# Kernel optimization log

Measured on AMD Instinct MI355X. Metric: run time of the kernel, lower is better.

The kernel has to match this reference:

```python
import jax, jax.numpy as jnp
import numpy as np
from jax import lax

SEQ, BATCH, IN, HID, OUT = 168, 4096, 24, 64, 9


def _uniform(key, shape, scale):
    return jax.random.uniform(key, shape, jnp.float32, -scale, scale)


def setup_inputs() -> dict:
    key = jax.random.key(0)
    ks = jax.random.split(key, 12)
    s = 1.0 / np.sqrt(HID)  # PyTorch LSTM/Linear init scale
    return {
        "x": jax.random.normal(ks[0], (SEQ, BATCH, IN), jnp.float32),
        # layer 0 LSTM (PyTorch gate order: i, f, g, o stacked along dim 0)
        "W_ih0": _uniform(ks[1], (4 * HID, IN), s),
        "W_hh0": _uniform(ks[2], (4 * HID, HID), s),
        "b_ih0": _uniform(ks[3], (4 * HID,), s),
        "b_hh0": _uniform(ks[4], (4 * HID,), s),
        # layer 1 LSTM
        "W_ih1": _uniform(ks[5], (4 * HID, HID), s),
        "W_hh1": _uniform(ks[6], (4 * HID, HID), s),
        "b_ih1": _uniform(ks[7], (4 * HID,), s),
        "b_hh1": _uniform(ks[8], (4 * HID,), s),
        # linear head
        "W_out": _uniform(ks[9], (OUT, HID), s),
        "b_out": _uniform(ks[10], (OUT,), s),
    }


def _lstm_layer(x, W_ih, W_hh, b_ih, b_hh):
    # x: [S, B, D]; returns hidden states [S, B, H]
    H = W_hh.shape[1]
    B = x.shape[1]
    # precompute input projections for all timesteps: [S, B, 4H]
    xg = jnp.einsum('sbd,gd->sbg', x, W_ih) + b_ih + b_hh

    def step(carry, xg_t):
        h, c = carry
        g = xg_t + h @ W_hh.T  # [B, 4H]
        i, f, gc, o = jnp.split(g, 4, axis=-1)
        c = jax.nn.sigmoid(f) * c + jax.nn.sigmoid(i) * jnp.tanh(gc)
        h = jax.nn.sigmoid(o) * jnp.tanh(c)
        return (h, c), h

    init = (jnp.zeros((B, H), x.dtype), jnp.zeros((B, H), x.dtype))
    _, hs = lax.scan(step, init, xg)
    return hs


def reference(x, W_ih0, W_hh0, b_ih0, b_hh0, W_ih1, W_hh1, b_ih1, b_hh1, W_out, b_out):
    h = _lstm_layer(x, W_ih0, W_hh0, b_ih0, b_hh0)   # [S, B, H]
    h = _lstm_layer(h, W_ih1, W_hh1, b_ih1, b_hh1)   # [S, B, H]
    out = jnp.einsum('sbh,oh->sbo', h, W_out) + b_out  # [S, B, OUT]
    return out
```

## Files before the change

### kernel.cpp

```cpp
#include <hip/hip_runtime.h>
#include <hip/hip_bf16.h>
#include <math.h>

#define SEQ   168
#define BATCH 4096
#define NOUT  9
#define NBLK  256

typedef short bf16x8 __attribute__((ext_vector_type(8)));
typedef float f32x4  __attribute__((ext_vector_type(4)));

#define MFMA(a,b,c) __builtin_amdgcn_mfma_f32_16x16x32_bf16((a),(b),(c),0,0,0)

static __device__ __forceinline__ float bf2f(unsigned short h){
    unsigned int u = ((unsigned int)h) << 16;
    return __builtin_bit_cast(float, u);
}
static __device__ __forceinline__ unsigned short f2bf(float f){
    return __builtin_bit_cast(unsigned short, __float2bfloat16(f));
}
static __device__ __forceinline__ void splitf(float f, unsigned short& hi, unsigned short& lo){
    hi = f2bf(f);
    float r = f - bf2f(hi);
    lo = (unsigned short)(__builtin_bit_cast(unsigned int, r) >> 16);
}
static __device__ __forceinline__ float sigf(float x){
    return __builtin_amdgcn_rcpf(1.0f + __expf(-x));
}
static __device__ __forceinline__ float tanhf_(float x){
    float r = __builtin_amdgcn_rcpf(1.0f + __expf(2.0f * x));
    return fmaf(-2.0f, r, 1.0f);
}
static __device__ __forceinline__ bf16x8 ldfrag(const unsigned short* p){
    const uint4 q = *reinterpret_cast<const uint4*>(p);
    return __builtin_bit_cast(bf16x8, q);
}

static __device__ __forceinline__ void gbar(int* cnt, int* phs, int* done,
                                            int tickval, int& ph, int lane){
    asm volatile("s_waitcnt lgkmcnt(0)" ::: "memory");
    if (lane == 0){
        int old = __hip_atomic_fetch_add(cnt, 1, __ATOMIC_ACQ_REL,
                                         __HIP_MEMORY_SCOPE_WORKGROUP);
        if (old == 3){
            *cnt = 0;
            __hip_atomic_store(done, tickval, __ATOMIC_RELEASE,
                               __HIP_MEMORY_SCOPE_WORKGROUP);
            __hip_atomic_store(phs, ph ^ 1, __ATOMIC_RELEASE,
                               __HIP_MEMORY_SCOPE_WORKGROUP);
        }
    }
    while (__hip_atomic_load(phs, __ATOMIC_ACQUIRE,
                             __HIP_MEMORY_SCOPE_WORKGROUP) == ph)
        __builtin_amdgcn_s_sleep(1);
    ph ^= 1;
}
static __device__ __forceinline__ void wait_ge(int* done, int need){
    if (__hip_atomic_load(done, __ATOMIC_ACQUIRE, __HIP_MEMORY_SCOPE_WORKGROUP) >= need) return;
    do { __builtin_amdgcn_s_sleep(1); }
    while (__hip_atomic_load(done, __ATOMIC_ACQUIRE, __HIP_MEMORY_SCOPE_WORKGROUP) < need);
}

__global__ __launch_bounds__(512, 2)
void lstm_fused(const float* __restrict__ x,
                const float* __restrict__ Wih0, const float* __restrict__ Whh0,
                const float* __restrict__ bih0, const float* __restrict__ bhh0,
                const float* __restrict__ Wih1, const float* __restrict__ Whh1,
                const float* __restrict__ bih1, const float* __restrict__ bhh1,
                const float* __restrict__ Wout, const float* __restrict__ bout,
                float* __restrict__ out)
{
    __shared__ __align__(16) unsigned short sXH[2][16][72];
    __shared__ __align__(16) unsigned short sH0H[2][16][72];
    __shared__ __align__(16) unsigned short sH1H[2][16][72];
    __shared__ int sync[8];

    const int tid  = threadIdx.x;
    const int half = tid >> 8;
    const int w2   = (tid >> 6) & 3;
    const int l    = tid & 63;
    const int lr   = l & 15;
    const int g    = l >> 4;
    const int r0   = blockIdx.x * 16;
    const int cg   = w2 * 16 + lr;

    if (tid < 8) sync[tid] = (tid >= 4) ? -1 : 0;

    for (int i = tid; i < (int)(2*16*72/2); i += 512){
        ((unsigned int*)sXH)[i]  = 0u;
        ((unsigned int*)sH0H)[i] = 0u;
        ((unsigned int*)sH1H)[i] = 0u;
    }
    __syncthreads();
    if (tid < 96){
        const float4 v = *reinterpret_cast<const float4*>(&x[(size_t)r0 * 24 + tid * 4]);
        const int row = (tid * 4) / 24, col = (tid * 4) % 24;
        ushort4 w = { f2bf(v.x), f2bf(v.y), f2bf(v.z), f2bf(v.w) };
        *reinterpret_cast<ushort4*>(&sXH[0][row][col]) = w;
    }
    __syncthreads();

    if (half == 0){
        bf16x8 B0H[4][3], B0L[4][3];
        #pragma unroll
        for (int gt = 0; gt < 4; ++gt){
            const int c = gt * 64 + cg;
            bf16x8 bh = {0,0,0,0,0,0,0,0}, bl = {0,0,0,0,0,0,0,0};
            if (g < 3){
                const float* pw = &Wih0[c * 24 + g * 8];
                #pragma unroll
                for (int j = 0; j < 8; ++j){ unsigned short hh, ll; splitf(pw[j], hh, ll); bh[j]=(short)hh; bl[j]=(short)ll; }
            }
            B0H[gt][0] = bh; B0L[gt][0] = bl;
            #pragma unroll
            for (int ks = 0; ks < 2; ++ks){
                bf16x8 ch, cl;
                const float* pw = &Whh0[c * 64 + ks * 32 + g * 8];
                #pragma unroll
                for (int j = 0; j < 8; ++j){ unsigned short hh, ll; splitf(pw[j], hh, ll); ch[j]=(short)hh; cl[j]=(short)ll; }
                B0H[gt][1+ks] = ch; B0L[gt][1+ks] = cl;
            }
        }
        float b0[4];
        #pragma unroll
        for (int gt = 0; gt < 4; ++gt) b0[gt] = bih0[gt*64 + cg] + bhh0[gt*64 + cg];

        const int oc = lr;
        bf16x8 WoH[2], WoL[2];
        #pragma unroll
        for (int tt = 0; tt < 2; ++tt){
            bf16x8 bh = {0,0,0,0,0,0,0,0}, bl = {0,0,0,0,0,0,0,0};
            if (oc < NOUT){
                const float* pw = &Wout[oc * 64 + tt * 32 + g * 8];
                #pragma unroll
                for (int j = 0; j < 8; ++j){ unsigned short hh, ll; splitf(pw[j], hh, ll); bh[j]=(short)hh; bl[j]=(short)ll; }
            }
            WoH[tt] = bh; WoL[tt] = bl;
        }
        const float bo0 = (oc < NOUT) ? bout[oc] : 0.f;
        float* houtp = out + (size_t)(r0 + g * 4) * NOUT + oc;

        const float* xfp = x + ((size_t)BATCH + r0) * 24 + tid * 4;
        float c0[4] = {0,0,0,0};
        int ph = 0;
        for (int t = 0; t < SEQ + 2; ++t){
            const int p = t & 1;
            const bool cmp = (t < SEQ);
            const bool ldx = (tid < 96) && (t + 1 < SEQ);
            float4 pref;
            if (ldx){ pref = *reinterpret_cast<const float4*>(xfp); xfp += (size_t)BATCH * 24; }

            unsigned short hh[4];
            if (cmp){
                const bf16x8 AxH = ldfrag(&sXH[p][lr][g*8]);
                bf16x8 A0H[2];
                #pragma unroll
                for (int ks = 0; ks < 2; ++ks)
                    A0H[ks] = ldfrag(&sH0H[p][lr][ks*32 + g*8]);

                f32x4 a0[4];
                #pragma unroll
                for (int gt = 0; gt < 4; ++gt){ f32x4 a = {b0[gt],b0[gt],b0[gt],b0[gt]}; a0[gt] = a; }
                #pragma unroll
                for (int gt = 0; gt < 4; ++gt) a0[gt] = MFMA(AxH, B0H[gt][0], a0[gt]);
                #pragma unroll
                for (int gt = 0; gt < 4; ++gt) a0[gt] = MFMA(AxH, B0L[gt][0], a0[gt]);
                #pragma unroll
                for (int ks = 0; ks < 2; ++ks){
                    #pragma unroll
                    for (int gt = 0; gt < 4; ++gt) a0[gt] = MFMA(A0H[ks], B0H[gt][1+ks], a0[gt]);
                    #pragma unroll
                    for (int gt = 0; gt < 4; ++gt) a0[gt] = MFMA(A0H[ks], B0L[gt][1+ks], a0[gt]);
                }
                #pragma unroll
                for (int i = 0; i < 4; ++i){
                    const float ig = sigf(a0[0][i]);
                    const float fg = sigf(a0[1][i]);
                    const float gg = tanhf_(a0[2][i]);
                    const float og = sigf(a0[3][i]);
                    c0[i] = fg * c0[i] + ig * gg;
                    hh[i] = f2bf(og * tanhf_(c0[i]));
                }
            }
            if (ldx){
                const int row = (tid * 4) / 24, col = (tid * 4) % 24;
                ushort4 w = { f2bf(pref.x), f2bf(pref.y), f2bf(pref.z), f2bf(pref.w) };
                *reinterpret_cast<ushort4*>(&sXH[p ^ 1][row][col]) = w;
            }
            if (t >= 2) wait_ge(&sync[5], t - 1);
            if (cmp){
                #pragma unroll
                for (int i = 0; i < 4; ++i)
                    sH0H[p ^ 1][g * 4 + i][cg] = hh[i];
            }
            if (t >= 2 && w2 == (t & 3)){
                bf16x8 A1H[2];
                #pragma unroll
                for (int tt = 0; tt < 2; ++tt)
                    A1H[tt] = ldfrag(&sH1H[p][lr][tt*32 + g*8]);
                f32x4 ha = {bo0, bo0, bo0, bo0};
                #pragma unroll
                for (int tt = 0; tt < 2; ++tt){
                    ha = MFMA(A1H[tt], WoH[tt], ha);
                    ha = MFMA(A1H[tt], WoL[tt], ha);
                }
                if (oc < NOUT){
                    #pragma unroll
                    for (int i = 0; i < 4; ++i)
                        houtp[(size_t)i * NOUT] = ha[i];
                }
            }
            if (t >= 2) houtp += (size_t)BATCH * NOUT;
            gbar(&sync[0], &sync[2], &sync[4], t, ph, l);
        }
    } else {
        bf16x8 B1H[4][4], B1L[4][4];
        #pragma unroll
        for (int gt = 0; gt < 4; ++gt){
            const int c = gt * 64 + cg;
            #pragma unroll
            for (int ks = 0; ks < 2; ++ks){
                bf16x8 ch, cl;
                const float* pw = &Wih1[c * 64 + ks * 32 + g * 8];
                #pragma unroll
                for (int j = 0; j < 8; ++j){ unsigned short hh, ll; splitf(pw[j], hh, ll); ch[j]=(short)hh; cl[j]=(short)ll; }
                B1H[gt][ks] = ch; B1L[gt][ks] = cl;
            }
            #pragma unroll
            for (int ks = 0; ks < 2; ++ks){
                bf16x8 ch, cl;
                const float* pw = &Whh1[c * 64 + ks * 32 + g * 8];
                #pragma unroll
                for (int j = 0; j < 8; ++j){ unsigned short hh, ll; splitf(pw[j], hh, ll); ch[j]=(short)hh; cl[j]=(short)ll; }
                B1H[gt][2+ks] = ch; B1L[gt][2+ks] = cl;
            }
        }
        float b1[4];
        #pragma unroll
        for (int gt = 0; gt < 4; ++gt) b1[gt] = bih1[gt*64 + cg] + bhh1[gt*64 + cg];

        float c1[4] = {0,0,0,0};
        int ph = 0;
        for (int t = 1; t <= SEQ; ++t){
            const int p = t & 1;
            bf16x8 A1H[2];
            #pragma unroll
            for (int ks = 0; ks < 2; ++ks)
                A1H[ks] = ldfrag(&sH1H[p][lr][ks*32 + g*8]);
            f32x4 a1[4];
            #pragma unroll
            for (int gt = 0; gt < 4; ++gt){ f32x4 a = {b1[gt],b1[gt],b1[gt],b1[gt]}; a1[gt] = a; }
            #pragma unroll
            for (int ks = 0; ks < 2; ++ks){
                #pragma unroll
                for (int gt = 0; gt < 4; ++gt) a1[gt] = MFMA(A1H[ks], B1H[gt][2+ks], a1[gt]);
                #pragma unroll
                for (int gt = 0; gt < 4; ++gt) a1[gt] = MFMA(A1H[ks], B1L[gt][2+ks], a1[gt]);
            }
            wait_ge(&sync[4], t - 1);
            bf16x8 A0H[2];
            #pragma unroll
            for (int ks = 0; ks < 2; ++ks)
                A0H[ks] = ldfrag(&sH0H[p][lr][ks*32 + g*8]);
            #pragma unroll
            for (int ks = 0; ks < 2; ++ks){
                #pragma unroll
                for (int gt = 0; gt < 4; ++gt) a1[gt] = MFMA(A0H[ks], B1H[gt][ks], a1[gt]);
                #pragma unroll
                for (int gt = 0; gt < 4; ++gt) a1[gt] = MFMA(A0H[ks], B1L[gt][ks], a1[gt]);
            }
            #pragma unroll
            for (int i = 0; i < 4; ++i){
                const float ig = sigf(a1[0][i]);
                const float fg = sigf(a1[1][i]);
                const float gg = tanhf_(a1[2][i]);
                const float og = sigf(a1[3][i]);
                c1[i] = fg * c1[i] + ig * gg;
                sH1H[p ^ 1][g * 4 + i][cg] = f2bf(og * tanhf_(c1[i]));
            }
            gbar(&sync[1], &sync[3], &sync[5], t, ph, l);
        }
    }
}

extern "C" void kernel_launch(void* const* d_in, const int* in_sizes, int n_in,
                              void* d_out, int out_size, void* d_ws, size_t ws_size,
                              hipStream_t stream)
{
    const float* x    = (const float*)d_in[0];
    const float* Wih0 = (const float*)d_in[1];
    const float* Whh0 = (const float*)d_in[2];
    const float* bih0 = (const float*)d_in[3];
    const float* bhh0 = (const float*)d_in[4];
    const float* Wih1 = (const float*)d_in[5];
    const float* Whh1 = (const float*)d_in[6];
    const float* bih1 = (const float*)d_in[7];
    const float* bhh1 = (const float*)d_in[8];
    const float* Wout = (const float*)d_in[9];
    const float* bout = (const float*)d_in[10];
    float* out = (float*)d_out;

    lstm_fused<<<NBLK, 512, 0, stream>>>(x, Wih0, Whh0, bih0, bhh0,
                                         Wih1, Whh1, bih1, bhh1,
                                         Wout, bout, out);
}
```

Baseline: 194.4 us.

## Replace coarse layer-1 barrier waits with fine-grained per-wave event counters

```diff
diff --git a/kernel.cpp b/kernel.cpp
--- a/kernel.cpp
+++ b/kernel.cpp
@@ -56,9 +56,14 @@
     ph ^= 1;
 }
 static __device__ __forceinline__ void wait_ge(int* done, int need){
-    if (__hip_atomic_load(done, __ATOMIC_ACQUIRE, __HIP_MEMORY_SCOPE_WORKGROUP) >= need) return;
-    do { __builtin_amdgcn_s_sleep(1); }
-    while (__hip_atomic_load(done, __ATOMIC_ACQUIRE, __HIP_MEMORY_SCOPE_WORKGROUP) < need);
+    while (__hip_atomic_load(done, __ATOMIC_ACQUIRE,
+                             __HIP_MEMORY_SCOPE_WORKGROUP) < need) { }
+}
+static __device__ __forceinline__ void post_evt(int* ctr, int lane){
+    asm volatile("s_waitcnt lgkmcnt(0)" ::: "memory");
+    if (lane == 0)
+        __hip_atomic_fetch_add(ctr, 1, __ATOMIC_ACQ_REL,
+                               __HIP_MEMORY_SCOPE_WORKGROUP);
 }
 
 __global__ __launch_bounds__(512, 2)
@@ -84,7 +89,7 @@
     const int r0   = blockIdx.x * 16;
     const int cg   = w2 * 16 + lr;
 
-    if (tid < 8) sync[tid] = (tid >= 4) ? -1 : 0;
+    if (tid < 8) sync[tid] = (tid == 4 || tid == 5) ? -1 : 0;
 
     for (int i = tid; i < (int)(2*16*72/2); i += 512){
         ((unsigned int*)sXH)[i]  = 0u;
@@ -181,29 +186,30 @@
                     c0[i] = fg * c0[i] + ig * gg;
                     hh[i] = f2bf(og * tanhf_(c0[i]));
                 }
+                if (t >= 2) wait_ge(&sync[6], 4 * (t - 1));
+                #pragma unroll
+                for (int i = 0; i < 4; ++i)
+                    sH0H[p ^ 1][g * 4 + i][cg] = hh[i];
             }
             if (ldx){
                 const int row = (tid * 4) / 24, col = (tid * 4) % 24;
                 ushort4 w = { f2bf(pref.x), f2bf(pref.y), f2bf(pref.z), f2bf(pref.w) };
                 *reinterpret_cast<ushort4*>(&sXH[p ^ 1][row][col]) = w;
             }
-            if (t >= 2) wait_ge(&sync[5], t - 1);
-            if (cmp){
-                #pragma unroll
-                for (int i = 0; i < 4; ++i)
-                    sH0H[p ^ 1][g * 4 + i][cg] = hh[i];
-            }
-            if (t >= 2 && w2 == (t & 3)){
-                bf16x8 A1H[2];
-                #pragma unroll
-                for (int tt = 0; tt < 2; ++tt)
-                    A1H[tt] = ldfrag(&sH1H[p][lr][tt*32 + g*8]);
+            const bool headw = (t >= 2) && (w2 == (t & 3));
+            bf16x8 A1H0, A1H1;
+            if (headw){
+                wait_ge(&sync[7], 4 * (t - 1));
+                A1H0 = ldfrag(&sH1H[p][lr][g*8]);
+                A1H1 = ldfrag(&sH1H[p][lr][32 + g*8]);
+            }
+            gbar(&sync[0], &sync[2], &sync[4], t, ph, l);
+            if (headw){
                 f32x4 ha = {bo0, bo0, bo0, bo0};
-                #pragma unroll
-                for (int tt = 0; tt < 2; ++tt){
-                    ha = MFMA(A1H[tt], WoH[tt], ha);
-                    ha = MFMA(A1H[tt], WoL[tt], ha);
-                }
+                ha = MFMA(A1H0, WoH[0], ha);
+                ha = MFMA(A1H0, WoL[0], ha);
+                ha = MFMA(A1H1, WoH[1], ha);
+                ha = MFMA(A1H1, WoL[1], ha);
                 if (oc < NOUT){
                     #pragma unroll
                     for (int i = 0; i < 4; ++i)
@@ -211,7 +217,6 @@
                 }
             }
             if (t >= 2) houtp += (size_t)BATCH * NOUT;
-            gbar(&sync[0], &sync[2], &sync[4], t, ph, l);
         }
     } else {
         bf16x8 B1H[4][4], B1L[4][4];
@@ -247,21 +252,23 @@
             #pragma unroll
             for (int ks = 0; ks < 2; ++ks)
                 A1H[ks] = ldfrag(&sH1H[p][lr][ks*32 + g*8]);
-            f32x4 a1[4];
-            #pragma unroll
-            for (int gt = 0; gt < 4; ++gt){ f32x4 a = {b1[gt],b1[gt],b1[gt],b1[gt]}; a1[gt] = a; }
-            #pragma unroll
-            for (int ks = 0; ks < 2; ++ks){
-                #pragma unroll
-                for (int gt = 0; gt < 4; ++gt) a1[gt] = MFMA(A1H[ks], B1H[gt][2+ks], a1[gt]);
-                #pragma unroll
-                for (int gt = 0; gt < 4; ++gt) a1[gt] = MFMA(A1H[ks], B1L[gt][2+ks], a1[gt]);
-            }
             wait_ge(&sync[4], t - 1);
             bf16x8 A0H[2];
             #pragma unroll
             for (int ks = 0; ks < 2; ++ks)
                 A0H[ks] = ldfrag(&sH0H[p][lr][ks*32 + g*8]);
+
+            f32x4 a1[4];
+            #pragma unroll
+            for (int gt = 0; gt < 4; ++gt){ f32x4 a = {b1[gt],b1[gt],b1[gt],b1[gt]}; a1[gt] = a; }
+            #pragma unroll
+            for (int ks = 0; ks < 2; ++ks){
+                #pragma unroll
+                for (int gt = 0; gt < 4; ++gt) a1[gt] = MFMA(A1H[ks], B1H[gt][2+ks], a1[gt]);
+                #pragma unroll
+                for (int gt = 0; gt < 4; ++gt) a1[gt] = MFMA(A1H[ks], B1L[gt][2+ks], a1[gt]);
+            }
+            post_evt(&sync[6], l);
             #pragma unroll
             for (int ks = 0; ks < 2; ++ks){
                 #pragma unroll
@@ -278,6 +285,7 @@
                 c1[i] = fg * c1[i] + ig * gg;
                 sH1H[p ^ 1][g * 4 + i][cg] = f2bf(og * tanhf_(c1[i]));
             }
+            post_evt(&sync[7], l);
             gbar(&sync[1], &sync[3], &sync[5], t, ph, l);
         }
     }
```

New measurement: 242.0 us. +24.5%, slower.

## Triple-buffer layer-0 hidden state and move output head to layer-1 half

Applied to the files above, without the earlier changes.

```diff
diff --git a/kernel.cpp b/kernel.cpp
--- a/kernel.cpp
+++ b/kernel.cpp
@@ -71,7 +71,7 @@
                 float* __restrict__ out)
 {
     __shared__ __align__(16) unsigned short sXH[2][16][72];
-    __shared__ __align__(16) unsigned short sH0H[2][16][72];
+    __shared__ __align__(16) unsigned short sH0H[3][16][72];
     __shared__ __align__(16) unsigned short sH1H[2][16][72];
     __shared__ int sync[8];
 
@@ -84,13 +84,14 @@
     const int r0   = blockIdx.x * 16;
     const int cg   = w2 * 16 + lr;
 
-    if (tid < 8) sync[tid] = (tid >= 4) ? -1 : 0;
+    if (tid < 8) sync[tid] = (tid == 4) ? -1 : 0;
 
     for (int i = tid; i < (int)(2*16*72/2); i += 512){
         ((unsigned int*)sXH)[i]  = 0u;
-        ((unsigned int*)sH0H)[i] = 0u;
         ((unsigned int*)sH1H)[i] = 0u;
     }
+    for (int i = tid; i < (int)(3*16*72/2); i += 512)
+        ((unsigned int*)sH0H)[i] = 0u;
     __syncthreads();
     if (tid < 96){
         const float4 v = *reinterpret_cast<const float4*>(&x[(size_t)r0 * 24 + tid * 4]);
@@ -125,6 +126,85 @@
         #pragma unroll
         for (int gt = 0; gt < 4; ++gt) b0[gt] = bih0[gt*64 + cg] + bhh0[gt*64 + cg];
 
+        const float* xfp = x + ((size_t)BATCH + r0) * 24 + tid * 4;
+        float c0[4] = {0,0,0,0};
+        int ph = 0;
+        int pw = 0, pr = 2;
+        for (int t = 0; t < SEQ; ++t){
+            const int px = t & 1;
+            const bool ldx = (tid < 96) && (t + 1 < SEQ);
+            float4 pref;
+            if (ldx){ pref = *reinterpret_cast<const float4*>(xfp); xfp += (size_t)BATCH * 24; }
+
+            const bf16x8 AxH = ldfrag(&sXH[px][lr][g*8]);
+            bf16x8 A0H[2];
+            #pragma unroll
+            for (int ks = 0; ks < 2; ++ks)
+                A0H[ks] = ldfrag(&sH0H[pr][lr][ks*32 + g*8]);
+
+            f32x4 a0[4];
+            #pragma unroll
+            for (int gt = 0; gt < 4; ++gt){ f32x4 a = {b0[gt],b0[gt],b0[gt],b0[gt]}; a0[gt] = a; }
+            #pragma unroll
+            for (int gt = 0; gt < 4; ++gt) a0[gt] = MFMA(AxH, B0H[gt][0], a0[gt]);
+            #pragma unroll
+            for (int gt = 0; gt < 4; ++gt) a0[gt] = MFMA(AxH, B0L[gt][0], a0[gt]);
+            #pragma unroll
+            for (int ks = 0; ks < 2; ++ks){
+                #pragma unroll
+                for (int gt = 0; gt < 4; ++gt) a0[gt] = MFMA(A0H[ks], B0H[gt][1+ks], a0[gt]);
+                #pragma unroll
+                for (int gt = 0; gt < 4; ++gt) a0[gt] = MFMA(A0H[ks], B0L[gt][1+ks], a0[gt]);
+            }
+            unsigned short hh[4];
+            #pragma unroll
+            for (int i = 0; i < 4; ++i){
+                const float ig = sigf(a0[0][i]);
+                const float fg = sigf(a0[1][i]);
+                const float gg = tanhf_(a0[2][i]);
+                const float og = sigf(a0[3][i]);
+                c0[i] = fg * c0[i] + ig * gg;
+                hh[i] = f2bf(og * tanhf_(c0[i]));
+            }
+            if (t >= 3) wait_ge(&sync[5], t - 2);
+            #pragma unroll
+            for (int i = 0; i < 4; ++i)
+                sH0H[pw][g * 4 + i][cg] = hh[i];
+            if (ldx){
+                const int row = (tid * 4) / 24, col = (tid * 4) % 24;
+                ushort4 w = { f2bf(pref.x), f2bf(pref.y), f2bf(pref.z), f2bf(pref.w) };
+                *reinterpret_cast<ushort4*>(&sXH[px ^ 1][row][col]) = w;
+            }
+            gbar(&sync[0], &sync[2], &sync[4], t, ph, l);
+            pw = (pw == 2) ? 0 : pw + 1;
+            pr = (pr == 2) ? 0 : pr + 1;
+        }
+    } else {
+        bf16x8 B1H[4][4], B1L[4][4];
+        #pragma unroll
+        for (int gt = 0; gt < 4; ++gt){
+            const int c = gt * 64 + cg;
+            #pragma unroll
+            for (int ks = 0; ks < 2; ++ks){
+                bf16x8 ch, cl;
+                const float* pw = &Wih1[c * 64 + ks * 32 + g * 8];
+                #pragma unroll
+                for (int j = 0; j < 8; ++j){ unsigned short hh, ll; splitf(pw[j], hh, ll); ch[j]=(short)hh; cl[j]=(short)ll; }
+                B1H[gt][ks] = ch; B1L[gt][ks] = cl;
+            }
+            #pragma unroll
+            for (int ks = 0; ks < 2; ++ks){
+                bf16x8 ch, cl;
+                const float* pw = &Whh1[c * 64 + ks * 32 + g * 8];
+                #pragma unroll
+                for (int j = 0; j < 8; ++j){ unsigned short hh, ll; splitf(pw[j], hh, ll); ch[j]=(short)hh; cl[j]=(short)ll; }
+                B1H[gt][2+ks] = ch; B1L[gt][2+ks] = cl;
+            }
+        }
+        float b1[4];
+        #pragma unroll
+        for (int gt = 0; gt < 4; ++gt) b1[gt] = bih1[gt*64 + cg] + bhh1[gt*64 + cg];
+
         const int oc = lr;
         bf16x8 WoH[2], WoL[2];
         #pragma unroll
@@ -140,70 +220,37 @@
         const float bo0 = (oc < NOUT) ? bout[oc] : 0.f;
         float* houtp = out + (size_t)(r0 + g * 4) * NOUT + oc;
 
-        const float* xfp = x + ((size_t)BATCH + r0) * 24 + tid * 4;
-        float c0[4] = {0,0,0,0};
+        float c1[4] = {0,0,0,0};
         int ph = 0;
-        for (int t = 0; t < SEQ + 2; ++t){
+        int pr0 = 0;
+        for (int t = 1; t <= SEQ; ++t){
             const int p = t & 1;
-            const bool cmp = (t < SEQ);
-            const bool ldx = (tid < 96) && (t + 1 < SEQ);
-            float4 pref;
-            if (ldx){ pref = *reinterpret_cast<const float4*>(xfp); xfp += (size_t)BATCH * 24; }
-
-            unsigned short hh[4];
-            if (cmp){
-                const bf16x8 AxH = ldfrag(&sXH[p][lr][g*8]);
-                bf16x8 A0H[2];
-                #pragma unroll
-                for (int ks = 0; ks < 2; ++ks)
-                    A0H[ks] = ldfrag(&sH0H[p][lr][ks*32 + g*8]);
-
-                f32x4 a0[4];
-                #pragma unroll
-                for (int gt = 0; gt < 4; ++gt){ f32x4 a = {b0[gt],b0[gt],b0[gt],b0[gt]}; a0[gt] = a; }
-                #pragma unroll
-                for (int gt = 0; gt < 4; ++gt) a0[gt] = MFMA(AxH, B0H[gt][0], a0[gt]);
-                #pragma unroll
-                for (int gt = 0; gt < 4; ++gt) a0[gt] = MFMA(AxH, B0L[gt][0], a0[gt]);
-                #pragma unroll
-                for (int ks = 0; ks < 2; ++ks){
-                    #pragma unroll
-                    for (int gt = 0; gt < 4; ++gt) a0[gt] = MFMA(A0H[ks], B0H[gt][1+ks], a0[gt]);
-                    #pragma unroll
-                    for (int gt = 0; gt < 4; ++gt) a0[gt] = MFMA(A0H[ks], B0L[gt][1+ks], a0[gt]);
-                }
-                #pragma unroll
-                for (int i = 0; i < 4; ++i){
-                    const float ig = sigf(a0[0][i]);
-                    const float fg = sigf(a0[1][i]);
-                    const float gg = tanhf_(a0[2][i]);
-                    const float og = sigf(a0[3][i]);
-                    c0[i] = fg * c0[i] + ig * gg;
-                    hh[i] = f2bf(og * tanhf_(c0[i]));
-                }
-            }
-            if (ldx){
-                const int row = (tid * 4) / 24, col = (tid * 4) % 24;
-                ushort4 w = { f2bf(pref.x), f2bf(pref.y), f2bf(pref.z), f2bf(pref.w) };
-                *reinterpret_cast<ushort4*>(&sXH[p ^ 1][row][col]) = w;
-            }
-            if (t >= 2) wait_ge(&sync[5], t - 1);
-            if (cmp){
-                #pragma unroll
-                for (int i = 0; i < 4; ++i)
-                    sH0H[p ^ 1][g * 4 + i][cg] = hh[i];
+            bf16x8 A1H[2];
+            #pragma unroll
+            for (int ks = 0; ks < 2; ++ks)
+                A1H[ks] = ldfrag(&sH1H[p][lr][ks*32 + g*8]);
+            wait_ge(&sync[4], t - 1);
+            bf16x8 A0H[2];
+            #pragma unroll
+            for (int ks = 0; ks < 2; ++ks)
+                A0H[ks] = ldfrag(&sH0H[pr0][lr][ks*32 + g*8]);
+
+            f32x4 a1[4];
+            #pragma unroll
+            for (int gt = 0; gt < 4; ++gt){ f32x4 a = {b1[gt],b1[gt],b1[gt],b1[gt]}; a1[gt] = a; }
+            #pragma unroll
+            for (int ks = 0; ks < 2; ++ks){
+                #pragma unroll
+                for (int gt = 0; gt < 4; ++gt) a1[gt] = MFMA(A1H[ks], B1H[gt][2+ks], a1[gt]);
+                #pragma unroll
+                for (int gt = 0; gt < 4; ++gt) a1[gt] = MFMA(A1H[ks], B1L[gt][2+ks], a1[gt]);
             }
             if (t >= 2 && w2 == (t & 3)){
-                bf16x8 A1H[2];
-                #pragma unroll
-                for (int tt = 0; tt < 2; ++tt)
-                    A1H[tt] = ldfrag(&sH1H[p][lr][tt*32 + g*8]);
                 f32x4 ha = {bo0, bo0, bo0, bo0};
-                #pragma unroll
-                for (int tt = 0; tt < 2; ++tt){
-                    ha = MFMA(A1H[tt], WoH[tt], ha);
-                    ha = MFMA(A1H[tt], WoL[tt], ha);
-                }
+                ha = MFMA(A1H[0], WoH[0], ha);
+                ha = MFMA(A1H[0], WoL[0], ha);
+                ha = MFMA(A1H[1], WoH[1], ha);
+                ha = MFMA(A1H[1], WoL[1], ha);
                 if (oc < NOUT){
                     #pragma unroll
                     for (int i = 0; i < 4; ++i)
@@ -211,57 +258,6 @@
                 }
             }
             if (t >= 2) houtp += (size_t)BATCH * NOUT;
-            gbar(&sync[0], &sync[2], &sync[4], t, ph, l);
-        }
-    } else {
-        bf16x8 B1H[4][4], B1L[4][4];
-        #pragma unroll
-        for (int gt = 0; gt < 4; ++gt){
-            const int c = gt * 64 + cg;
-            #pragma unroll
-            for (int ks = 0; ks < 2; ++ks){
-                bf16x8 ch, cl;
-                const float* pw = &Wih1[c * 64 + ks * 32 + g * 8];
-                #pragma unroll
-                for (int j = 0; j < 8; ++j){ unsigned short hh, ll; splitf(pw[j], hh, ll); ch[j]=(short)hh; cl[j]=(short)ll; }
-                B1H[gt][ks] = ch; B1L[gt][ks] = cl;
-            }
-            #pragma unroll
-            for (int ks = 0; ks < 2; ++ks){
-                bf16x8 ch, cl;
-                const float* pw = &Whh1[c * 64 + ks * 32 + g * 8];
-                #pragma unroll
-                for (int j = 0; j < 8; ++j){ unsigned short hh, ll; splitf(pw[j], hh, ll); ch[j]=(short)hh; cl[j]=(short)ll; }
-                B1H[gt][2+ks] = ch; B1L[gt][2+ks] = cl;
-            }
-        }
-        float b1[4];
-        #pragma unroll
-        for (int gt = 0; gt < 4; ++gt) b1[gt] = bih1[gt*64 + cg] + bhh1[gt*64 + cg];
-
-        float c1[4] = {0,0,0,0};
-        int ph = 0;
-        for (int t = 1; t <= SEQ; ++t){
-            const int p = t & 1;
-            bf16x8 A1H[2];
-            #pragma unroll
-            for (int ks = 0; ks < 2; ++ks)
-                A1H[ks] = ldfrag(&sH1H[p][lr][ks*32 + g*8]);
-            f32x4 a1[4];
-            #pragma unroll
-            for (int gt = 0; gt < 4; ++gt){ f32x4 a = {b1[gt],b1[gt],b1[gt],b1[gt]}; a1[gt] = a; }
-            #pragma unroll
-            for (int ks = 0; ks < 2; ++ks){
-                #pragma unroll
-                for (int gt = 0; gt < 4; ++gt) a1[gt] = MFMA(A1H[ks], B1H[gt][2+ks], a1[gt]);
-                #pragma unroll
-                for (int gt = 0; gt < 4; ++gt) a1[gt] = MFMA(A1H[ks], B1L[gt][2+ks], a1[gt]);
-            }
-            wait_ge(&sync[4], t - 1);
-            bf16x8 A0H[2];
-            #pragma unroll
-            for (int ks = 0; ks < 2; ++ks)
-                A0H[ks] = ldfrag(&sH0H[p][lr][ks*32 + g*8]);
             #pragma unroll
             for (int ks = 0; ks < 2; ++ks){
                 #pragma unroll
@@ -279,6 +275,24 @@
                 sH1H[p ^ 1][g * 4 + i][cg] = f2bf(og * tanhf_(c1[i]));
             }
             gbar(&sync[1], &sync[3], &sync[5], t, ph, l);
+            pr0 = (pr0 == 2) ? 0 : pr0 + 1;
+        }
+        {
+            const int pe = (SEQ + 1) & 1;
+            if (w2 == ((SEQ + 1) & 3)){
+                bf16x8 A1H0 = ldfrag(&sH1H[pe][lr][g*8]);
+                bf16x8 A1H1 = ldfrag(&sH1H[pe][lr][32 + g*8]);
+                f32x4 ha = {bo0, bo0, bo0, bo0};
+                ha = MFMA(A1H0, WoH[0], ha);
+                ha = MFMA(A1H0, WoL[0], ha);
+                ha = MFMA(A1H1, WoH[1], ha);
+                ha = MFMA(A1H1, WoL[1], ha);
+                if (oc < NOUT){
+                    #pragma unroll
+                    for (int i = 0; i < 4; ++i)
+                        houtp[(size_t)i * NOUT] = ha[i];
+                }
+            }
         }
     }
 }
```

Result: faster. 186.8 us (-3.9%).
